# Optimization experiments

Hardware: AMD Instinct MI355X
Metric: run time of the kernel (lower is better)

## Reference

```python
import jax, jax.numpy as jnp
import numpy as np

EPS = 1e-5

def _ln(x):
    # LayerNorm over last dim, no affine (elementwise_affine=False)
    mu = jnp.mean(x, axis=-1, keepdims=True)
    var = jnp.mean(jnp.square(x - mu), axis=-1, keepdims=True)
    return (x - mu) * jax.lax.rsqrt(var + EPS)

def setup_inputs() -> dict:
    key = jax.random.key(0)
    ks = jax.random.split(key, 6)
    B, L, D = 2, 2048, 2048
    s = 1.0 / np.sqrt(D)
    return {
        "x": jax.random.normal(ks[0], (B, L, D), jnp.float32),
        "Wq": jax.random.normal(ks[1], (D, D), jnp.float32) * s,
        "Wk": jax.random.normal(ks[2], (D, D), jnp.float32) * s,
        "Wv": jax.random.normal(ks[3], (D, D), jnp.float32) * s,
        "Wo": jax.random.normal(ks[4], (D, D), jnp.float32) * s,
        "bo": jnp.zeros((D,), jnp.float32),
    }

def reference(x, Wq, Wk, Wv, Wo, bo):
    B, L, D = x.shape
    H = 16
    hd = D // H
    q = (x @ Wq.T).reshape(B, L, H, hd)
    k = (x @ Wk.T).reshape(B, L, H, hd)
    v = (x @ Wv.T).reshape(B, L, H, hd)
    q = _ln(q)
    k = _ln(k)
    scores = jnp.einsum('blhd,bshd->bhls', q, k) / np.sqrt(hd)
    causal = jnp.tril(jnp.ones((L, L), bool))  # [L, L]
    scores = jnp.where(causal[None, None], scores, -jnp.inf)
    probs = jax.nn.softmax(scores, axis=-1)
    out = jnp.einsum('bhls,bshd->blhd', probs, v).reshape(B, L, D)
    return out @ Wo.T + bo
```

## Files before the change

### kernel.cpp

```cpp
#include <hip/hip_runtime.h>
#include <stdint.h>

typedef unsigned short u16;
typedef __attribute__((ext_vector_type(8))) unsigned short u16x8;
typedef __attribute__((ext_vector_type(8))) __bf16 bf16x8;
typedef __attribute__((ext_vector_type(4))) float f32x4;
typedef __attribute__((ext_vector_type(8))) float f32x8;

#define AS_G __attribute__((address_space(1)))
#define AS_L __attribute__((address_space(3)))

static __device__ __forceinline__ void gload_lds16(const u16* g, u16* l) {
  __builtin_amdgcn_global_load_lds((AS_G void*)(u16*)g, (AS_L void*)l, 16, 0, 0);
}

static __device__ __forceinline__ u16 f2bf(float f) {
  union { float f; unsigned u; } v; v.f = f;
  return (u16)((v.u + 0x7FFFu + ((v.u >> 16) & 1u)) >> 16);
}
static __device__ __forceinline__ float bf2f(u16 b) {
  union { unsigned u; float f; } v; v.u = ((unsigned)b) << 16;
  return v.f;
}
static __device__ __forceinline__ u16 f2bf_trunc(float f) {
  union { float f; unsigned u; } v; v.f = f;
  return (u16)(v.u >> 16);
}

#define BAR() do { asm volatile("" ::: "memory"); __builtin_amdgcn_s_barrier(); asm volatile("" ::: "memory"); } while (0)

__global__ __launch_bounds__(256) void cast_all(
    const float* __restrict__ x, const float* __restrict__ Wq,
    const float* __restrict__ Wk, const float* __restrict__ Wv,
    const float* __restrict__ Wo,
    u16* __restrict__ xb, u16* __restrict__ Wcat, u16* __restrict__ Wob)
{
  const int NX = (4096 * 2048) / 8;
  const int NW = (2048 * 2048) / 8;
  const int total = NX + 4 * NW;
  for (int i = blockIdx.x * 256 + threadIdx.x; i < total; i += gridDim.x * 256) {
    const float* src; u16* dst; int idx;
    if (i < NX)               { src = x;  dst = xb;                 idx = i; }
    else if (i < NX + NW)     { src = Wq; dst = Wcat;               idx = i - NX; }
    else if (i < NX + 2*NW)   { src = Wk; dst = Wcat + 2048*2048;   idx = i - NX - NW; }
    else if (i < NX + 3*NW)   { src = Wv; dst = Wcat + 2*2048*2048; idx = i - NX - 2*NW; }
    else                      { src = Wo; dst = Wob;                idx = i - NX - 3*NW; }
    f32x8 v = *(const f32x8*)(src + (size_t)idx * 8);
    u16x8 o;
    #pragma unroll
    for (int e = 0; e < 8; e++) o[e] = f2bf(v[e]);
    *(u16x8*)(dst + (size_t)idx * 8) = o;
  }
}

#define MFMA2(q, x00, x01, x10, x11) \
  do { __builtin_amdgcn_s_setprio(1); \
    _Pragma("unroll") \
    for (int nf = 0; nf < 4; ++nf) { \
      acc[2*(q)][nf]   = __builtin_amdgcn_mfma_f32_16x16x32_bf16(x00, breg[nf][0], acc[2*(q)][nf], 0, 0, 0); \
      acc[2*(q)][nf]   = __builtin_amdgcn_mfma_f32_16x16x32_bf16(x01, breg[nf][1], acc[2*(q)][nf], 0, 0, 0); \
      acc[2*(q)+1][nf] = __builtin_amdgcn_mfma_f32_16x16x32_bf16(x10, breg[nf][0], acc[2*(q)+1][nf], 0, 0, 0); \
      acc[2*(q)+1][nf] = __builtin_amdgcn_mfma_f32_16x16x32_bf16(x11, breg[nf][1], acc[2*(q)+1][nf], 0, 0, 0); \
    } \
    __builtin_amdgcn_s_setprio(0); } while (0)

__global__ __launch_bounds__(512, 2) void gemm256(
    const u16* __restrict__ A, const u16* __restrict__ B,
    u16* __restrict__ Cout, int M, int N, int K)
{
  __shared__ u16 As[2][256 * 64];
  __shared__ u16 Bs[2][256 * 64];
  const int tid = threadIdx.x, lane = tid & 63, wid = tid >> 6;
  const int wm = wid >> 2, wn = wid & 3;
  const int row0 = blockIdx.y * 256, col0 = blockIdx.x * 256;
  const int NT = K >> 6;

  const int sr  = tid >> 3;
  const int scb = ((tid & 7) * 16) ^ ((sr & 7) << 4);

  auto stA = [&](int buf, int t, int half) {
    const u16* src = A + (size_t)(row0 + half * 128 + sr) * K + t * 64 + (scb >> 1);
    u16* dst = As[buf] + half * 8192 + wid * 512;
    gload_lds16(src, dst);
    gload_lds16(src + (size_t)64 * K, dst + 4096);
  };
  auto stB = [&](int buf, int t, int half) {
    const u16* src = B + (size_t)(col0 + half * 128 + sr) * K + t * 64 + (scb >> 1);
    u16* dst = Bs[buf] + half * 8192 + wid * 512;
    gload_lds16(src, dst);
    gload_lds16(src + (size_t)64 * K, dst + 4096);
  };
  auto ldA = [&](int buf, int mf, int k) {
    int ra = wm * 128 + mf * 16 + (lane & 15);
    int bc = (k * 64 + ((lane >> 4) << 4)) ^ ((ra & 7) << 4);
    return *(const bf16x8*)((const char*)As[buf] + ra * 128 + bc);
  };
  auto ldB = [&](int buf, int nf, int k) {
    int rb = wn * 64 + nf * 16 + (lane & 15);
    int bc = (k * 64 + ((lane >> 4) << 4)) ^ ((rb & 7) << 4);
    return *(const bf16x8*)((const char*)Bs[buf] + rb * 128 + bc);
  };

  f32x4 acc[8][4] = {};
  bf16x8 breg[4][2];

  stA(0, 0, 0); stA(0, 0, 1); stB(0, 0, 0); stB(0, 0, 1);
  stB(1, 1, 0); stB(1, 1, 1);
  asm volatile("s_waitcnt vmcnt(4)" ::: "memory");
  BAR();

  for (int it = 0; it < NT / 2; ++it) {
    const int t1  = 2 * it + 1;
    const int pf0 = (2 * it + 2 < NT) ? (2 * it + 2) : (NT - 1);
    const int pf1 = (2 * it + 3 < NT) ? (2 * it + 3) : (NT - 1);
    #pragma unroll
    for (int hf = 0; hf < 2; ++hf) {
      const int cb = hf;
      #pragma unroll
      for (int nf = 0; nf < 4; ++nf) {
        breg[nf][0] = ldB(cb, nf, 0);
        breg[nf][1] = ldB(cb, nf, 1);
      }
      bf16x8 a00 = ldA(cb, 0, 0), a01 = ldA(cb, 0, 1);
      bf16x8 a10 = ldA(cb, 1, 0), a11 = ldA(cb, 1, 1);
      BAR();
      if (hf == 0) stA(1, t1, 0); else stA(0, pf0, 0);
      MFMA2(0, a00, a01, a10, a11);
      a00 = ldA(cb, 2, 0); a01 = ldA(cb, 2, 1);
      a10 = ldA(cb, 3, 0); a11 = ldA(cb, 3, 1);
      BAR();
      if (hf == 0) stA(1, t1, 1); else stA(0, pf0, 1);
      MFMA2(1, a00, a01, a10, a11);
      a00 = ldA(cb, 4, 0); a01 = ldA(cb, 4, 1);
      a10 = ldA(cb, 5, 0); a11 = ldA(cb, 5, 1);
      BAR();
      if (hf == 0) stB(0, pf0, 0); else stB(1, pf1, 0);
      MFMA2(2, a00, a01, a10, a11);
      a00 = ldA(cb, 6, 0); a01 = ldA(cb, 6, 1);
      a10 = ldA(cb, 7, 0); a11 = ldA(cb, 7, 1);
      BAR();
      if (hf == 0) stB(0, pf0, 1); else stB(1, pf1, 1);
      MFMA2(3, a00, a01, a10, a11);
      asm volatile("s_waitcnt vmcnt(4)" ::: "memory");
      BAR();
    }
  }
  asm volatile("s_waitcnt vmcnt(0)" ::: "memory");
  BAR();

  if (col0 < 4096) {
    float* red = (float*)As;
    #pragma unroll
    for (int mf = 0; mf < 8; ++mf) {
      #pragma unroll
      for (int e = 0; e < 4; ++e) {
        float s = acc[mf][0][e] + acc[mf][1][e] + acc[mf][2][e] + acc[mf][3][e];
        float q = acc[mf][0][e]*acc[mf][0][e] + acc[mf][1][e]*acc[mf][1][e]
                + acc[mf][2][e]*acc[mf][2][e] + acc[mf][3][e]*acc[mf][3][e];
        #pragma unroll
        for (int m = 1; m < 16; m <<= 1) { s += __shfl_xor(s, m); q += __shfl_xor(q, m); }
        if ((lane & 15) == 0) {
          int rl = mf * 16 + (lane >> 4) * 4 + e;
          red[wid * 256 + rl * 2]     = s;
          red[wid * 256 + rl * 2 + 1] = q;
        }
      }
    }
    BAR();
    const float mul = (col0 < 2048) ? (0.08838834764831845f * 1.4426950408889634f) : 1.0f;
    #pragma unroll
    for (int mf = 0; mf < 8; ++mf) {
      #pragma unroll
      for (int e = 0; e < 4; ++e) {
        int rl = mf * 16 + (lane >> 4) * 4 + e;
        float s = red[wid * 256 + rl * 2]     + red[(wid ^ 1) * 256 + rl * 2];
        float q = red[wid * 256 + rl * 2 + 1] + red[(wid ^ 1) * 256 + rl * 2 + 1];
        float mu = s * (1.f / 128.f);
        float var = q * (1.f / 128.f) - mu * mu;
        float rstd = rsqrtf(var + 1e-5f) * mul;
        int r = row0 + wm * 128 + rl;
        #pragma unroll
        for (int nf = 0; nf < 4; ++nf) {
          int c = col0 + wn * 64 + nf * 16 + (lane & 15);
          Cout[(size_t)r * N + c] = f2bf((acc[mf][nf][e] - mu) * rstd);
        }
      }
    }
  } else {
    #pragma unroll
    for (int mf = 0; mf < 8; ++mf) {
      #pragma unroll
      for (int nf = 0; nf < 4; ++nf) {
        #pragma unroll
        for (int e = 0; e < 4; ++e) {
          int r = row0 + wm * 128 + mf * 16 + (lane >> 4) * 4 + e;
          int c = col0 + wn * 64 + nf * 16 + (lane & 15);
          Cout[(size_t)r * N + c] = f2bf(acc[mf][nf][e]);
        }
      }
    }
  }
}

__global__ __launch_bounds__(512, 2) void gemm_ao(
    const u16* __restrict__ A, const u16* __restrict__ B,
    float* __restrict__ C, const float* __restrict__ bias,
    int M, int N, int K)
{
  __shared__ u16 As[2][256 * 64];
  __shared__ u16 Bs[2][128 * 64];
  const int tid = threadIdx.x, lane = tid & 63, wid = tid >> 6;
  const int wm = wid >> 1, wn = wid & 1;
  const int row0 = blockIdx.y * 256, col0 = blockIdx.x * 128;
  const int NT = K >> 6;

  const int sr  = tid >> 3;
  const int scb = ((tid & 7) * 16) ^ ((sr & 7) << 4);

  auto stA = [&](int buf, int t, int u) {
    const u16* src = A + (size_t)(row0 + u * 64 + sr) * K + t * 64 + (scb >> 1);
    gload_lds16(src, As[buf] + u * 4096 + wid * 512);
  };
  auto stB = [&](int buf, int t, int u) {
    const u16* src = B + (size_t)(col0 + u * 64 + sr) * K + t * 64 + (scb >> 1);
    gload_lds16(src, Bs[buf] + u * 4096 + wid * 512);
  };
  auto ldA = [&](int buf, int mf, int k) {
    int ra = wm * 64 + mf * 16 + (lane & 15);
    int bc = (k * 64 + ((lane >> 4) << 4)) ^ ((ra & 7) << 4);
    return *(const bf16x8*)((const char*)As[buf] + ra * 128 + bc);
  };
  auto ldB = [&](int buf, int nf, int k) {
    int rb = wn * 64 + nf * 16 + (lane & 15);
    int bc = (k * 64 + ((lane >> 4) << 4)) ^ ((rb & 7) << 4);
    return *(const bf16x8*)((const char*)Bs[buf] + rb * 128 + bc);
  };

  f32x4 acc[4][4] = {};
  bf16x8 breg[4][2];

  stA(0, 0, 0); stA(0, 0, 1); stA(0, 0, 2); stA(0, 0, 3);
  stB(0, 0, 0); stB(0, 0, 1);
  stB(1, 1, 0); stB(1, 1, 1);
  asm volatile("s_waitcnt vmcnt(2)" ::: "memory");
  BAR();

  for (int it = 0; it < NT / 2; ++it) {
    const int t1  = 2 * it + 1;
    const int pf0 = (2 * it + 2 < NT) ? (2 * it + 2) : (NT - 1);
    const int pf1 = (2 * it + 3 < NT) ? (2 * it + 3) : (NT - 1);
    #pragma unroll
    for (int hf = 0; hf < 2; ++hf) {
      const int cb = hf;
      #pragma unroll
      for (int nf = 0; nf < 4; ++nf) { breg[nf][0] = ldB(cb, nf, 0); breg[nf][1] = ldB(cb, nf, 1); }
      bf16x8 a0 = ldA(cb, 0, 0), a1 = ldA(cb, 0, 1);
      BAR();
      if (hf == 0) { stA(1, t1, 0); stA(1, t1, 1); } else { stA(0, pf0, 0); stA(0, pf0, 1); }
      __builtin_amdgcn_s_setprio(1);
      #pragma unroll
      for (int nf = 0; nf < 4; ++nf) {
        acc[0][nf] = __builtin_amdgcn_mfma_f32_16x16x32_bf16(a0, breg[nf][0], acc[0][nf], 0, 0, 0);
        acc[0][nf] = __builtin_amdgcn_mfma_f32_16x16x32_bf16(a1, breg[nf][1], acc[0][nf], 0, 0, 0);
      }
      __builtin_amdgcn_s_setprio(0);
      bf16x8 b0 = ldA(cb, 1, 0), b1 = ldA(cb, 1, 1);
      bf16x8 c0 = ldA(cb, 2, 0), c1 = ldA(cb, 2, 1);
      BAR();
      if (hf == 0) { stA(1, t1, 2); stA(1, t1, 3); } else { stA(0, pf0, 2); stA(0, pf0, 3); }
      __builtin_amdgcn_s_setprio(1);
      #pragma unroll
      for (int nf = 0; nf < 4; ++nf) {
        acc[1][nf] = __builtin_amdgcn_mfma_f32_16x16x32_bf16(b0, breg[nf][0], acc[1][nf], 0, 0, 0);
        acc[1][nf] = __builtin_amdgcn_mfma_f32_16x16x32_bf16(b1, breg[nf][1], acc[1][nf], 0, 0, 0);
        acc[2][nf] = __builtin_amdgcn_mfma_f32_16x16x32_bf16(c0, breg[nf][0], acc[2][nf], 0, 0, 0);
        acc[2][nf] = __builtin_amdgcn_mfma_f32_16x16x32_bf16(c1, breg[nf][1], acc[2][nf], 0, 0, 0);
      }
      __builtin_amdgcn_s_setprio(0);
      a0 = ldA(cb, 3, 0); a1 = ldA(cb, 3, 1);
      BAR();
      if (hf == 0) { stB(0, pf0, 0); stB(0, pf0, 1); } else { stB(1, pf1, 0); stB(1, pf1, 1); }
      __builtin_amdgcn_s_setprio(1);
      #pragma unroll
      for (int nf = 0; nf < 4; ++nf) {
        acc[3][nf] = __builtin_amdgcn_mfma_f32_16x16x32_bf16(a0, breg[nf][0], acc[3][nf], 0, 0, 0);
        acc[3][nf] = __builtin_amdgcn_mfma_f32_16x16x32_bf16(a1, breg[nf][1], acc[3][nf], 0, 0, 0);
      }
      __builtin_amdgcn_s_setprio(0);
      asm volatile("s_waitcnt vmcnt(2)" ::: "memory");
      BAR();
    }
  }
  asm volatile("s_waitcnt vmcnt(0)" ::: "memory");

  #pragma unroll
  for (int mf = 0; mf < 4; ++mf) {
    #pragma unroll
    for (int nf = 0; nf < 4; ++nf) {
      #pragma unroll
      for (int e = 0; e < 4; ++e) {
        int r = row0 + wm * 64 + mf * 16 + (lane >> 4) * 4 + e;
        int c = col0 + wn * 64 + nf * 16 + (lane & 15);
        C[(size_t)r * N + c] = acc[mf][nf][e] + bias[c];
      }
    }
  }
}

__global__ __launch_bounds__(256) void transpose_v(const u16* __restrict__ QKV, u16* __restrict__ Vt)
{
  __shared__ u16 T[64 * 65];
  const int d0 = blockIdx.x * 64;
  const int l0 = blockIdx.y * 64;
  const int bh = blockIdx.z;
  const int b = bh >> 4, h = bh & 15;
  const int t = threadIdx.x;
  #pragma unroll
  for (int i = 0; i < 2; i++) {
    int c = t + i * 256;
    int l = c >> 3, dc = (c & 7) * 8;
    u16x8 v = *(const u16x8*)(QKV + (size_t)(b*2048 + l0 + l) * 6144 + 4096 + h*128 + d0 + dc);
    #pragma unroll
    for (int e = 0; e < 8; e++) T[l * 65 + dc + e] = v[e];
  }
  __syncthreads();
  #pragma unroll
  for (int i = 0; i < 2; i++) {
    int c = t + i * 256;
    int d = c >> 3, lc = (c & 7) * 8;
    u16x8 o;
    #pragma unroll
    for (int e = 0; e < 8; e++) o[e] = T[(lc + e) * 65 + d];
    *(u16x8*)(Vt + (size_t)((b*16 + h) * 128 + d0 + d) * 2048 + l0 + lc) = o;
  }
}

static __device__ __forceinline__ void stage_k_tile(
    const u16* __restrict__ QKV, int b, int h, int j0, u16* Kbuf, int tid, int wid)
{
  #pragma unroll
  for (int i = 0; i < 4; i++) {
    int c = i * 256 + tid;
    int r = c >> 4, ob = (c & 15) * 16;
    int cb = ob ^ ((r & 7) << 4);
    const u16* g = QKV + (size_t)(b*2048 + j0 + r) * 6144 + 2048 + h*128 + (cb >> 1);
    gload_lds16(g, Kbuf + (i * 256 + wid * 64) * 8);
  }
}
static __device__ __forceinline__ void stage_v_tile(
    const u16* __restrict__ Vt, int b, int h, int j0, u16* Vbuf, int tid, int wid)
{
  #pragma unroll
  for (int i = 0; i < 4; i++) {
    int c = i * 256 + tid;
    int r = c >> 3, ob = (c & 7) * 16;
    int cb = ob ^ ((r & 7) << 4);
    const u16* g = Vt + (size_t)((b*16 + h) * 128 + r) * 2048 + j0 + (cb >> 1);
    gload_lds16(g, Vbuf + (i * 256 + wid * 64) * 8);
  }
}

__global__ __launch_bounds__(256) void attn(
    const u16* __restrict__ QKV, const u16* __restrict__ Vt, u16* __restrict__ AO)
{
  const int flat = blockIdx.x + (blockIdx.y << 4) + (blockIdx.z << 8);
  const int swz = (flat & 7) * 64 + (flat >> 3);
  const int pair = swz & 15;
  const int h = (swz >> 4) & 15;
  const int b = swz >> 8;
  const int tid = threadIdx.x, lane = tid & 63, wid = tid >> 6;

  __shared__ u16 Ks[2][64 * 128];
  __shared__ u16 Vs[2][128 * 64];
  __shared__ u16 Ps[4][16 * 64];

  for (int side = 0; side < 2; side++) {
    const int pp = side ? (31 - pair) : pair;
    const int l0 = pp * 64;
    const int ntile = pp + 1;

    bf16x8 qa[4];
    const u16* qrow = QKV + (size_t)(b*2048 + l0 + wid*16 + (lane & 15)) * 6144
                      + h*128 + (lane >> 4) * 8;
    #pragma unroll
    for (int ks = 0; ks < 4; ks++) qa[ks] = *(const bf16x8*)(qrow + ks * 32);

    f32x4 o[8] = {};
    float mrun[4] = {-1e30f, -1e30f, -1e30f, -1e30f};
    float lrun[4] = {};

    stage_v_tile(Vt, b, h, 0, Vs[0], tid, wid);
    stage_k_tile(QKV, b, h, 0, Ks[0], tid, wid);
    int cur = 0;

    for (int t = 0; t < ntile; t++) {
      if (t + 1 < ntile) {
        stage_v_tile(Vt, b, h, (t + 1) * 64, Vs[cur ^ 1], tid, wid);
        stage_k_tile(QKV, b, h, (t + 1) * 64, Ks[cur ^ 1], tid, wid);
        asm volatile("s_waitcnt vmcnt(8)" ::: "memory");
      } else {
        asm volatile("s_waitcnt vmcnt(0)" ::: "memory");
      }
      __builtin_amdgcn_s_barrier();
      asm volatile("" ::: "memory");

      f32x4 s[4] = {};
      const char* Kc = (const char*)Ks[cur];
      __builtin_amdgcn_s_setprio(1);
      #pragma unroll
      for (int nt = 0; nt < 4; nt++) {
        #pragma unroll
        for (int ks = 0; ks < 4; ks++) {
          int r = nt * 16 + (lane & 15);
          int cb = ks * 64 + (lane >> 4) * 16;
          bf16x8 kb = *(const bf16x8*)(Kc + r * 256 + (cb ^ ((lane & 7) << 4)));
          s[nt] = __builtin_amdgcn_mfma_f32_16x16x32_bf16(qa[ks], kb, s[nt], 0, 0, 0);
        }
      }
      __builtin_amdgcn_s_setprio(0);

      if (t == ntile - 1) {
        #pragma unroll
        for (int nt = 0; nt < 4; nt++) {
          #pragma unroll
          for (int e = 0; e < 4; e++) {
            int i_loc = wid * 16 + (lane >> 4) * 4 + e;
            int j_loc = nt * 16 + (lane & 15);
            if (j_loc > i_loc) s[nt][e] = -1e30f;
          }
        }
      }

      float pmax[4];
      #pragma unroll
      for (int e = 0; e < 4; e++) {
        float v = fmaxf(fmaxf(s[0][e], s[1][e]), fmaxf(s[2][e], s[3][e]));
        v = fmaxf(v, __shfl_xor(v, 1));
        v = fmaxf(v, __shfl_xor(v, 2));
        v = fmaxf(v, __shfl_xor(v, 4));
        v = fmaxf(v, __shfl_xor(v, 8));
        pmax[e] = v;
      }
      bool need = (pmax[0] > mrun[0] + 8.f) || (pmax[1] > mrun[1] + 8.f) ||
                  (pmax[2] > mrun[2] + 8.f) || (pmax[3] > mrun[3] + 8.f);
      if (__any(need)) {
        float alpha[4];
        #pragma unroll
        for (int e = 0; e < 4; e++) {
          float mi = fmaxf(mrun[e], pmax[e]);
          alpha[e] = exp2f(mrun[e] - mi);
          mrun[e] = mi;
          lrun[e] *= alpha[e];
        }
        #pragma unroll
        for (int dt = 0; dt < 8; dt++)
          #pragma unroll
          for (int e = 0; e < 4; e++)
            o[dt][e] *= alpha[e];
      }

      char* PsW = (char*)Ps[wid];
      #pragma unroll
      for (int nt = 0; nt < 4; nt++) {
        #pragma unroll
        for (int e = 0; e < 4; e++) {
          float p = exp2f(s[nt][e] - mrun[e]);
          lrun[e] += p;
          int i_ = (lane >> 4) * 4 + e;
          int jb = (nt * 16 + (lane & 15)) * 2;
          *(u16*)(PsW + i_ * 128 + (jb ^ ((i_ & 7) << 4))) = f2bf_trunc(p);
        }
      }

      const char* Vc = (const char*)Vs[cur];
      __builtin_amdgcn_s_setprio(1);
      #pragma unroll
      for (int ks = 0; ks < 2; ks++) {
        int ir = lane & 15;
        int jb = ks * 64 + (lane >> 4) * 16;
        bf16x8 pa = *(const bf16x8*)(PsW + ir * 128 + (jb ^ ((ir & 7) << 4)));
        #pragma unroll
        for (int dt = 0; dt < 8; dt++) {
          int dr = dt * 16 + (lane & 15);
          bf16x8 vb = *(const bf16x8*)(Vc + dr * 128 + (jb ^ ((lane & 7) << 4)));
          o[dt] = __builtin_amdgcn_mfma_f32_16x16x32_bf16(pa, vb, o[dt], 0, 0, 0);
        }
      }
      __builtin_amdgcn_s_setprio(0);

      asm volatile("s_waitcnt lgkmcnt(0)" ::: "memory");
      __builtin_amdgcn_s_barrier();
      asm volatile("" ::: "memory");
      cur ^= 1;
    }

    #pragma unroll
    for (int e = 0; e < 4; e++) {
      float l = lrun[e];
      l += __shfl_xor(l, 1);
      l += __shfl_xor(l, 2);
      l += __shfl_xor(l, 4);
      l += __shfl_xor(l, 8);
      float inv = 1.0f / l;
      int rglob = b * 2048 + l0 + wid * 16 + (lane >> 4) * 4 + e;
      #pragma unroll
      for (int dt = 0; dt < 8; dt++)
        AO[(size_t)rglob * 2048 + h * 128 + dt * 16 + (lane & 15)] = f2bf(o[dt][e] * inv);
    }
  }
}

extern "C" void kernel_launch(void* const* d_in, const int* in_sizes, int n_in,
                              void* d_out, int out_size, void* d_ws, size_t ws_size,
                              hipStream_t stream)
{
  const float* x  = (const float*)d_in[0];
  const float* Wq = (const float*)d_in[1];
  const float* Wk = (const float*)d_in[2];
  const float* Wv = (const float*)d_in[3];
  const float* Wo = (const float*)d_in[4];
  const float* bo = (const float*)d_in[5];

  char* ws = (char*)d_ws;
  u16* xb   = (u16*)(ws);
  u16* Wcat = (u16*)(ws + 16777216);
  u16* Wob  = (u16*)(ws + 16777216 + 25165824);
  u16* QKV  = (u16*)(ws + 16777216 + 25165824 + 8388608);
  u16* AO   = xb;
  u16* Vt   = Wcat;

  cast_all<<<dim3(2048), dim3(256), 0, stream>>>(x, Wq, Wk, Wv, Wo, xb, Wcat, Wob);
  gemm256<<<dim3(24, 16), dim3(512), 0, stream>>>(xb, Wcat, QKV, 4096, 6144, 2048);
  transpose_v<<<dim3(2, 32, 32), dim3(256), 0, stream>>>(QKV, Vt);
  attn<<<dim3(16, 16, 2), dim3(256), 0, stream>>>(QKV, Vt, AO);
  gemm_ao<<<dim3(16, 16), dim3(512), 0, stream>>>(AO, Wob, (float*)d_out, bo, 4096, 2048, 2048);
}
```

Measured before the change: 279.9 us.

## Fuse V transpose into QKV GEMM epilogue and retile to 128x256

Removes the separate transpose_v kernel. The QKV GEMM now writes V directly in transposed layout through an LDS staging buffer in its epilogue, and writes only Q/K into a narrower buffer. The GEMM tile changes from 256x256 to 128x256 with launch bounds of one block per CU, which doubles the grid to 768 blocks. This cuts one launch and a full read/write pass over V, at the cost of less data reuse per tile and a changed occupancy profile.

```diff
diff --git a/kernel.cpp b/kernel.cpp
--- a/kernel.cpp
+++ b/kernel.cpp
@@ -53,59 +53,55 @@
   }
 }
 
-#define MFMA2(q, x00, x01, x10, x11) \
+__global__ __launch_bounds__(512, 1) void gemm_qkv(
+    const u16* __restrict__ A, const u16* __restrict__ B,
+    u16* __restrict__ QK, u16* __restrict__ Vt, int K)
+{
+  __shared__ char SM[98304];
+  u16* Asb = (u16*)SM;
+  u16* Bsb = (u16*)(SM + 32768);
+  const int tid = threadIdx.x, lane = tid & 63, wid = tid >> 6;
+  const int wm = wid >> 2, wn = wid & 3;
+  const int row0 = blockIdx.x * 128, col0 = blockIdx.y * 256;
+  const int NT = K >> 6;
+
+  const int sr  = tid >> 3;
+  const int scb = ((tid & 7) * 16) ^ ((sr & 7) << 4);
+
+  auto stA = [&](int buf, int t, int u) {
+    const u16* src = A + (size_t)(row0 + u * 64 + sr) * K + t * 64 + (scb >> 1);
+    gload_lds16(src, Asb + buf * 8192 + u * 4096 + wid * 512);
+  };
+  auto stB = [&](int buf, int t, int u) {
+    const u16* src = B + (size_t)(col0 + u * 64 + sr) * K + t * 64 + (scb >> 1);
+    gload_lds16(src, Bsb + buf * 16384 + u * 4096 + wid * 512);
+  };
+  auto ldA = [&](int buf, int mf, int k) {
+    int ra = wm * 64 + mf * 16 + (lane & 15);
+    int bc = (k * 64 + ((lane >> 4) << 4)) ^ ((ra & 7) << 4);
+    return *(const bf16x8*)((const char*)Asb + buf * 16384 + ra * 128 + bc);
+  };
+  auto ldB = [&](int buf, int nf, int k) {
+    int rb = wn * 64 + nf * 16 + (lane & 15);
+    int bc = (k * 64 + ((lane >> 4) << 4)) ^ ((rb & 7) << 4);
+    return *(const bf16x8*)((const char*)Bsb + buf * 32768 + rb * 128 + bc);
+  };
+
+  f32x4 acc[4][4] = {};
+  bf16x8 breg[4][2];
+
+#define MFMA_PH(mf, x0, x1) \
   do { __builtin_amdgcn_s_setprio(1); \
     _Pragma("unroll") \
     for (int nf = 0; nf < 4; ++nf) { \
-      acc[2*(q)][nf]   = __builtin_amdgcn_mfma_f32_16x16x32_bf16(x00, breg[nf][0], acc[2*(q)][nf], 0, 0, 0); \
-      acc[2*(q)][nf]   = __builtin_amdgcn_mfma_f32_16x16x32_bf16(x01, breg[nf][1], acc[2*(q)][nf], 0, 0, 0); \
-      acc[2*(q)+1][nf] = __builtin_amdgcn_mfma_f32_16x16x32_bf16(x10, breg[nf][0], acc[2*(q)+1][nf], 0, 0, 0); \
-      acc[2*(q)+1][nf] = __builtin_amdgcn_mfma_f32_16x16x32_bf16(x11, breg[nf][1], acc[2*(q)+1][nf], 0, 0, 0); \
+      acc[mf][nf] = __builtin_amdgcn_mfma_f32_16x16x32_bf16(x0, breg[nf][0], acc[mf][nf], 0, 0, 0); \
+      acc[mf][nf] = __builtin_amdgcn_mfma_f32_16x16x32_bf16(x1, breg[nf][1], acc[mf][nf], 0, 0, 0); \
     } \
     __builtin_amdgcn_s_setprio(0); } while (0)
 
-__global__ __launch_bounds__(512, 2) void gemm256(
-    const u16* __restrict__ A, const u16* __restrict__ B,
-    u16* __restrict__ Cout, int M, int N, int K)
-{
-  __shared__ u16 As[2][256 * 64];
-  __shared__ u16 Bs[2][256 * 64];
-  const int tid = threadIdx.x, lane = tid & 63, wid = tid >> 6;
-  const int wm = wid >> 2, wn = wid & 3;
-  const int row0 = blockIdx.y * 256, col0 = blockIdx.x * 256;
-  const int NT = K >> 6;
-
-  const int sr  = tid >> 3;
-  const int scb = ((tid & 7) * 16) ^ ((sr & 7) << 4);
-
-  auto stA = [&](int buf, int t, int half) {
-    const u16* src = A + (size_t)(row0 + half * 128 + sr) * K + t * 64 + (scb >> 1);
-    u16* dst = As[buf] + half * 8192 + wid * 512;
-    gload_lds16(src, dst);
-    gload_lds16(src + (size_t)64 * K, dst + 4096);
-  };
-  auto stB = [&](int buf, int t, int half) {
-    const u16* src = B + (size_t)(col0 + half * 128 + sr) * K + t * 64 + (scb >> 1);
-    u16* dst = Bs[buf] + half * 8192 + wid * 512;
-    gload_lds16(src, dst);
-    gload_lds16(src + (size_t)64 * K, dst + 4096);
-  };
-  auto ldA = [&](int buf, int mf, int k) {
-    int ra = wm * 128 + mf * 16 + (lane & 15);
-    int bc = (k * 64 + ((lane >> 4) << 4)) ^ ((ra & 7) << 4);
-    return *(const bf16x8*)((const char*)As[buf] + ra * 128 + bc);
-  };
-  auto ldB = [&](int buf, int nf, int k) {
-    int rb = wn * 64 + nf * 16 + (lane & 15);
-    int bc = (k * 64 + ((lane >> 4) << 4)) ^ ((rb & 7) << 4);
-    return *(const bf16x8*)((const char*)Bs[buf] + rb * 128 + bc);
-  };
-
-  f32x4 acc[8][4] = {};
-  bf16x8 breg[4][2];
-
-  stA(0, 0, 0); stA(0, 0, 1); stB(0, 0, 0); stB(0, 0, 1);
-  stB(1, 1, 0); stB(1, 1, 1);
+  stA(0, 0, 0); stA(0, 0, 1);
+  stB(0, 0, 0); stB(0, 0, 1); stB(0, 0, 2); stB(0, 0, 3);
+  stB(1, 1, 0); stB(1, 1, 1); stB(1, 1, 2); stB(1, 1, 3);
   asm volatile("s_waitcnt vmcnt(4)" ::: "memory");
   BAR();
 
@@ -117,30 +113,21 @@
     for (int hf = 0; hf < 2; ++hf) {
       const int cb = hf;
       #pragma unroll
-      for (int nf = 0; nf < 4; ++nf) {
-        breg[nf][0] = ldB(cb, nf, 0);
-        breg[nf][1] = ldB(cb, nf, 1);
-      }
-      bf16x8 a00 = ldA(cb, 0, 0), a01 = ldA(cb, 0, 1);
-      bf16x8 a10 = ldA(cb, 1, 0), a11 = ldA(cb, 1, 1);
-      BAR();
-      if (hf == 0) stA(1, t1, 0); else stA(0, pf0, 0);
-      MFMA2(0, a00, a01, a10, a11);
-      a00 = ldA(cb, 2, 0); a01 = ldA(cb, 2, 1);
-      a10 = ldA(cb, 3, 0); a11 = ldA(cb, 3, 1);
-      BAR();
-      if (hf == 0) stA(1, t1, 1); else stA(0, pf0, 1);
-      MFMA2(1, a00, a01, a10, a11);
-      a00 = ldA(cb, 4, 0); a01 = ldA(cb, 4, 1);
-      a10 = ldA(cb, 5, 0); a11 = ldA(cb, 5, 1);
-      BAR();
-      if (hf == 0) stB(0, pf0, 0); else stB(1, pf1, 0);
-      MFMA2(2, a00, a01, a10, a11);
-      a00 = ldA(cb, 6, 0); a01 = ldA(cb, 6, 1);
-      a10 = ldA(cb, 7, 0); a11 = ldA(cb, 7, 1);
-      BAR();
-      if (hf == 0) stB(0, pf0, 1); else stB(1, pf1, 1);
-      MFMA2(3, a00, a01, a10, a11);
+      for (int nf = 0; nf < 4; ++nf) { breg[nf][0] = ldB(cb, nf, 0); breg[nf][1] = ldB(cb, nf, 1); }
+      bf16x8 a0 = ldA(cb, 0, 0), a1 = ldA(cb, 0, 1);
+      BAR();
+      if (hf == 0) { stA(1, t1, 0); stA(1, t1, 1); } else { stA(0, pf0, 0); stA(0, pf0, 1); }
+      MFMA_PH(0, a0, a1);
+      a0 = ldA(cb, 1, 0); a1 = ldA(cb, 1, 1);
+      BAR();
+      if (hf == 0) { stB(0, pf0, 0); stB(0, pf0, 1); } else { stB(1, pf1, 0); stB(1, pf1, 1); }
+      MFMA_PH(1, a0, a1);
+      a0 = ldA(cb, 2, 0); a1 = ldA(cb, 2, 1);
+      BAR();
+      if (hf == 0) { stB(0, pf0, 2); stB(0, pf0, 3); } else { stB(1, pf1, 2); stB(1, pf1, 3); }
+      MFMA_PH(2, a0, a1);
+      a0 = ldA(cb, 3, 0); a1 = ldA(cb, 3, 1);
+      MFMA_PH(3, a0, a1);
       asm volatile("s_waitcnt vmcnt(4)" ::: "memory");
       BAR();
     }
@@ -149,9 +136,9 @@
   BAR();
 
   if (col0 < 4096) {
-    float* red = (float*)As;
-    #pragma unroll
-    for (int mf = 0; mf < 8; ++mf) {
+    float* red = (float*)SM;
+    #pragma unroll
+    for (int mf = 0; mf < 4; ++mf) {
       #pragma unroll
       for (int e = 0; e < 4; ++e) {
         float s = acc[mf][0][e] + acc[mf][1][e] + acc[mf][2][e] + acc[mf][3][e];
@@ -161,45 +148,58 @@
         for (int m = 1; m < 16; m <<= 1) { s += __shfl_xor(s, m); q += __shfl_xor(q, m); }
         if ((lane & 15) == 0) {
           int rl = mf * 16 + (lane >> 4) * 4 + e;
-          red[wid * 256 + rl * 2]     = s;
-          red[wid * 256 + rl * 2 + 1] = q;
+          red[wid * 128 + rl * 2]     = s;
+          red[wid * 128 + rl * 2 + 1] = q;
         }
       }
     }
     BAR();
     const float mul = (col0 < 2048) ? (0.08838834764831845f * 1.4426950408889634f) : 1.0f;
     #pragma unroll
-    for (int mf = 0; mf < 8; ++mf) {
+    for (int mf = 0; mf < 4; ++mf) {
       #pragma unroll
       for (int e = 0; e < 4; ++e) {
         int rl = mf * 16 + (lane >> 4) * 4 + e;
-        float s = red[wid * 256 + rl * 2]     + red[(wid ^ 1) * 256 + rl * 2];
-        float q = red[wid * 256 + rl * 2 + 1] + red[(wid ^ 1) * 256 + rl * 2 + 1];
+        float s = red[wid * 128 + rl * 2]     + red[(wid ^ 1) * 128 + rl * 2];
+        float q = red[wid * 128 + rl * 2 + 1] + red[(wid ^ 1) * 128 + rl * 2 + 1];
         float mu = s * (1.f / 128.f);
         float var = q * (1.f / 128.f) - mu * mu;
         float rstd = rsqrtf(var + 1e-5f) * mul;
-        int r = row0 + wm * 128 + rl;
+        int r = row0 + wm * 64 + rl;
         #pragma unroll
         for (int nf = 0; nf < 4; ++nf) {
           int c = col0 + wn * 64 + nf * 16 + (lane & 15);
-          Cout[(size_t)r * N + c] = f2bf((acc[mf][nf][e] - mu) * rstd);
+          QK[(size_t)r * 4096 + c] = f2bf((acc[mf][nf][e] - mu) * rstd);
         }
       }
     }
   } else {
-    #pragma unroll
-    for (int mf = 0; mf < 8; ++mf) {
+    u16* T = (u16*)SM;
+    #pragma unroll
+    for (int mf = 0; mf < 4; ++mf) {
       #pragma unroll
       for (int nf = 0; nf < 4; ++nf) {
         #pragma unroll
         for (int e = 0; e < 4; ++e) {
-          int r = row0 + wm * 128 + mf * 16 + (lane >> 4) * 4 + e;
-          int c = col0 + wn * 64 + nf * 16 + (lane & 15);
-          Cout[(size_t)r * N + c] = f2bf(acc[mf][nf][e]);
-        }
-      }
-    }
-  }
+          int r = wm * 64 + mf * 16 + (lane >> 4) * 4 + e;
+          int c = wn * 64 + nf * 16 + (lane & 15);
+          T[c * 136 + r] = f2bf(acc[mf][nf][e]);
+        }
+      }
+    }
+    BAR();
+    const int dr = tid >> 1, half = tid & 1;
+    const int dg = col0 - 4096 + dr;
+    const int h = dg >> 7, dd = dg & 127;
+    const int b = row0 >> 11;
+    const int lb = (row0 & 2047) + half * 64;
+    u16* dst = Vt + ((size_t)((b * 16 + h) * 128 + dd)) * 2048 + lb;
+    const u16* srcT = T + dr * 136 + half * 64;
+    #pragma unroll
+    for (int j = 0; j < 8; ++j)
+      *(u16x8*)(dst + j * 8) = *(const u16x8*)(srcT + j * 8);
+  }
+#undef MFMA_PH
 }
 
 __global__ __launch_bounds__(512, 2) void gemm_ao(
@@ -307,43 +307,15 @@
   }
 }
 
-__global__ __launch_bounds__(256) void transpose_v(const u16* __restrict__ QKV, u16* __restrict__ Vt)
-{
-  __shared__ u16 T[64 * 65];
-  const int d0 = blockIdx.x * 64;
-  const int l0 = blockIdx.y * 64;
-  const int bh = blockIdx.z;
-  const int b = bh >> 4, h = bh & 15;
-  const int t = threadIdx.x;
-  #pragma unroll
-  for (int i = 0; i < 2; i++) {
-    int c = t + i * 256;
-    int l = c >> 3, dc = (c & 7) * 8;
-    u16x8 v = *(const u16x8*)(QKV + (size_t)(b*2048 + l0 + l) * 6144 + 4096 + h*128 + d0 + dc);
-    #pragma unroll
-    for (int e = 0; e < 8; e++) T[l * 65 + dc + e] = v[e];
-  }
-  __syncthreads();
-  #pragma unroll
-  for (int i = 0; i < 2; i++) {
-    int c = t + i * 256;
-    int d = c >> 3, lc = (c & 7) * 8;
-    u16x8 o;
-    #pragma unroll
-    for (int e = 0; e < 8; e++) o[e] = T[(lc + e) * 65 + d];
-    *(u16x8*)(Vt + (size_t)((b*16 + h) * 128 + d0 + d) * 2048 + l0 + lc) = o;
-  }
-}
-
 static __device__ __forceinline__ void stage_k_tile(
-    const u16* __restrict__ QKV, int b, int h, int j0, u16* Kbuf, int tid, int wid)
+    const u16* __restrict__ QK, int b, int h, int j0, u16* Kbuf, int tid, int wid)
 {
   #pragma unroll
   for (int i = 0; i < 4; i++) {
     int c = i * 256 + tid;
     int r = c >> 4, ob = (c & 15) * 16;
     int cb = ob ^ ((r & 7) << 4);
-    const u16* g = QKV + (size_t)(b*2048 + j0 + r) * 6144 + 2048 + h*128 + (cb >> 1);
+    const u16* g = QK + (size_t)(b*2048 + j0 + r) * 4096 + 2048 + h*128 + (cb >> 1);
     gload_lds16(g, Kbuf + (i * 256 + wid * 64) * 8);
   }
 }
@@ -361,7 +333,7 @@
 }
 
 __global__ __launch_bounds__(256) void attn(
-    const u16* __restrict__ QKV, const u16* __restrict__ Vt, u16* __restrict__ AO)
+    const u16* __restrict__ QK, const u16* __restrict__ Vt, u16* __restrict__ AO)
 {
   const int flat = blockIdx.x + (blockIdx.y << 4) + (blockIdx.z << 8);
   const int swz = (flat & 7) * 64 + (flat >> 3);
@@ -380,7 +352,7 @@
     const int ntile = pp + 1;
 
     bf16x8 qa[4];
-    const u16* qrow = QKV + (size_t)(b*2048 + l0 + wid*16 + (lane & 15)) * 6144
+    const u16* qrow = QK + (size_t)(b*2048 + l0 + wid*16 + (lane & 15)) * 4096
                       + h*128 + (lane >> 4) * 8;
     #pragma unroll
     for (int ks = 0; ks < 4; ks++) qa[ks] = *(const bf16x8*)(qrow + ks * 32);
@@ -390,13 +362,13 @@
     float lrun[4] = {};
 
     stage_v_tile(Vt, b, h, 0, Vs[0], tid, wid);
-    stage_k_tile(QKV, b, h, 0, Ks[0], tid, wid);
+    stage_k_tile(QK, b, h, 0, Ks[0], tid, wid);
     int cur = 0;
 
     for (int t = 0; t < ntile; t++) {
       if (t + 1 < ntile) {
         stage_v_tile(Vt, b, h, (t + 1) * 64, Vs[cur ^ 1], tid, wid);
-        stage_k_tile(QKV, b, h, (t + 1) * 64, Ks[cur ^ 1], tid, wid);
+        stage_k_tile(QK, b, h, (t + 1) * 64, Ks[cur ^ 1], tid, wid);
         asm volatile("s_waitcnt vmcnt(8)" ::: "memory");
       } else {
         asm volatile("s_waitcnt vmcnt(0)" ::: "memory");
@@ -525,13 +497,12 @@
   u16* xb   = (u16*)(ws);
   u16* Wcat = (u16*)(ws + 16777216);
   u16* Wob  = (u16*)(ws + 16777216 + 25165824);
-  u16* QKV  = (u16*)(ws + 16777216 + 25165824 + 8388608);
+  u16* QK   = (u16*)(ws + 16777216 + 25165824 + 8388608);
+  u16* Vt   = (u16*)(ws + 16777216 + 25165824 + 8388608 + 33554432);
   u16* AO   = xb;
-  u16* Vt   = Wcat;
 
   cast_all<<<dim3(2048), dim3(256), 0, stream>>>(x, Wq, Wk, Wv, Wo, xb, Wcat, Wob);
-  gemm256<<<dim3(24, 16), dim3(512), 0, stream>>>(xb, Wcat, QKV, 4096, 6144, 2048);
-  transpose_v<<<dim3(2, 32, 32), dim3(256), 0, stream>>>(QKV, Vt);
-  attn<<<dim3(16, 16, 2), dim3(256), 0, stream>>>(QKV, Vt, AO);
+  gemm_qkv<<<dim3(32, 24), dim3(512), 0, stream>>>(xb, Wcat, QK, Vt, 2048);
+  attn<<<dim3(16, 16, 2), dim3(256), 0, stream>>>(QK, Vt, AO);
   gemm_ao<<<dim3(16, 16), dim3(512), 0, stream>>>(AO, Wob, (float*)d_out, bo, 4096, 2048, 2048);
 }
```

New measurement: 258.9 us. 1.08x faster.
